# Optimization experiments

Measured on AMD Instinct MI355X. Metric: run time of the kernel, lower is better.

The kernel has to match this reference:

```python
import jax, jax.numpy as jnp
import numpy as np

B, C, H, W = 16, 512, 56, 56
K = 8            # downsample factor
HEADS = 8
EXP = 3          # attn_expansion (int)
HID = HEADS * EXP  # DLA hidden channels = 24
HEAD_DIM = C // HEADS
SCALE = HEAD_DIM ** -0.5
N = H * W
NK = (H // K) * (W // K)
EPS = 1e-5


def conv2d(x, w, stride=1, padding='VALID', groups=1):
    # x: NCHW, w: OIHW
    return jax.lax.conv_general_dilated(
        x, w, (stride, stride), padding,
        dimension_numbers=('NCHW', 'OIHW', 'NCHW'),
        feature_group_count=groups)


def group_norm(x, scale, bias, groups):
    b, c, h, w = x.shape
    xg = x.reshape(b, groups, c // groups, h, w)
    mu = xg.mean(axis=(2, 3, 4), keepdims=True)
    var = xg.var(axis=(2, 3, 4), keepdims=True)
    xg = (xg - mu) * jax.lax.rsqrt(var + EPS)
    x = xg.reshape(b, c, h, w)
    return x * scale[None, :, None, None] + bias[None, :, None, None]


def swish(x):
    return x * jax.nn.sigmoid(x)


def setup_inputs() -> dict:
    key = jax.random.key(0)
    ks = jax.random.split(key, 12)
    s = 0.02
    return {
        'x': jax.random.normal(ks[0], (B, C, H, W), jnp.float32),
        'q_w': jax.random.normal(ks[1], (C, C), jnp.float32) * s,
        'down_w': jax.random.normal(ks[2], (C, 1, K, K), jnp.float32) * s,  # depthwise
        'kv_w': jax.random.normal(ks[3], (C, 2 * C), jnp.float32) * s,
        'proj_w': jax.random.normal(ks[4], (C, C), jnp.float32) * s,
        'proj_b': jnp.zeros((C,), jnp.float32),
        'rel_bias': jax.random.normal(ks[5], (N, NK), jnp.float32) * s,
        'expand_w': jax.random.normal(ks[6], (HID, HEADS, 1, 1), jnp.float32) * s,
        'gn1_s': jnp.ones((HID,), jnp.float32), 'gn1_b': jnp.zeros((HID,), jnp.float32),
        'dw_w': jax.random.normal(ks[7], (HID, 1, 3, 3), jnp.float32) * s,
        'gn2_s': jnp.ones((HID,), jnp.float32), 'gn2_b': jnp.zeros((HID,), jnp.float32),
        'reduce_w': jax.random.normal(ks[8], (HEADS, HID, 1, 1), jnp.float32) * s,
        'gn3_s': jnp.ones((HEADS,), jnp.float32), 'gn3_b': jnp.zeros((HEADS,), jnp.float32),
    }


def dla(a, expand_w, gn1_s, gn1_b, dw_w, gn2_s, gn2_b, reduce_w, gn3_s, gn3_b):
    # a: (B, HEADS, N, NK) treated as NCHW image
    a = swish(group_norm(conv2d(a, expand_w), gn1_s, gn1_b, EXP))
    a = swish(group_norm(conv2d(a, dw_w, padding='SAME', groups=HID), gn2_s, gn2_b, EXP))
    a = group_norm(conv2d(a, reduce_w), gn3_s, gn3_b, 1)
    return a


def reference(x, q_w, down_w, kv_w, proj_w, proj_b, rel_bias,
              expand_w, gn1_s, gn1_b, dw_w, gn2_s, gn2_b,
              reduce_w, gn3_s, gn3_b):
    b = x.shape[0]
    # downsampled kv: depthwise conv kernel=stride=K
    kvx = conv2d(x, down_w, stride=K, groups=C)           # (B, C, H/K, W/K)
    kvx = kvx.reshape(b, C, NK).transpose(0, 2, 1)        # (B, NK, C)
    kv = kvx @ kv_w                                       # (B, NK, 2C)
    kv = kv.reshape(b, NK, 2, HEADS, HEAD_DIM).transpose(2, 0, 3, 1, 4)
    k, v = kv[0], kv[1]                                   # (B, heads, NK, hd)
    q = (x.reshape(b, C, N).transpose(0, 2, 1) @ q_w)     # (B, N, C)
    q = q.reshape(b, N, HEADS, HEAD_DIM).transpose(0, 2, 1, 3)  # (B, heads, N, hd)
    attn = jnp.einsum('bhnd,bhmd->bhnm', q, k) * SCALE + rel_bias
    attn = jax.nn.softmax(attn, axis=-1)
    attn = dla(attn, expand_w, gn1_s, gn1_b, dw_w, gn2_s, gn2_b,
               reduce_w, gn3_s, gn3_b)
    out = jnp.einsum('bhnm,bhmd->bhnd', attn, v)          # (B, heads, N, hd)
    out = out.transpose(0, 2, 1, 3).reshape(b, N, C)      # (B, N, C)
    out = out @ proj_w + proj_b
    # faithful to torch: raw reshape (B, N, C) -> (B, C, H, W), no transpose
    return out.reshape(b, C, H, W)
```

## Files before the change

kernel.cpp:

```cpp
#include <hip/hip_runtime.h>
#include <hip/hip_bf16.h>
#include <stdint.h>

#define B_    16
#define C_    512
#define HIMG  56
#define N_    3136
#define NK_   49
#define NH_   8
#define HD_   64
#define JP_   52
#define J_    416
#define HID_  24
#define MP_   50
#define POS_  153664
#define CNT_  1229312.0f
#define EPS_  1e-5f
#define SCALE_ 0.125f

typedef __attribute__((ext_vector_type(8))) short short8;
typedef __attribute__((ext_vector_type(4))) float floatx4;

static __device__ __forceinline__ uint16_t f2bf(float f) {
  uint32_t u = __builtin_bit_cast(uint32_t, f);
  u = (u + 0x7FFFu + ((u >> 16) & 1u)) >> 16;
  return (uint16_t)u;
}
static __device__ __forceinline__ float bf2f(uint16_t h) {
  uint32_t u = ((uint32_t)h) << 16;
  return __builtin_bit_cast(float, u);
}
static __device__ __forceinline__ uint16_t f2h(float f) {
  _Float16 h = (_Float16)f;
  return __builtin_bit_cast(uint16_t, h);
}
static __device__ __forceinline__ float h2f(uint16_t u) {
  return (float)__builtin_bit_cast(_Float16, u);
}
static __device__ __forceinline__ float swishf(float z) {
  return z * __builtin_amdgcn_rcpf(1.f + __expf(-z));
}
static __device__ __forceinline__ void ld_h8(const uint16_t* p, float* a) {
  uint4 v = *(const uint4*)p;
  a[0] = h2f((uint16_t)(v.x & 0xFFFFu)); a[1] = h2f((uint16_t)(v.x >> 16));
  a[2] = h2f((uint16_t)(v.y & 0xFFFFu)); a[3] = h2f((uint16_t)(v.y >> 16));
  a[4] = h2f((uint16_t)(v.z & 0xFFFFu)); a[5] = h2f((uint16_t)(v.z >> 16));
  a[6] = h2f((uint16_t)(v.w & 0xFFFFu)); a[7] = h2f((uint16_t)(v.w >> 16));
}

static __device__ __forceinline__ void gn1_affine(const float* __restrict__ moms,
    const float* __restrict__ ew, const float* __restrict__ gs,
    const float* __restrict__ gb, int b, int g, float* al, float* be) {
  float m1[8];
#pragma unroll
  for (int h = 0; h < 8; ++h) m1[h] = moms[b * 44 + h];
  float sum = 0.f, ssq = 0.f;
#pragma unroll
  for (int o2 = 0; o2 < 8; ++o2) {
    int o = g * 8 + o2;
    float e[8];
#pragma unroll
    for (int h = 0; h < 8; ++h) e[h] = ew[o * 8 + h];
    float so = 0.f;
#pragma unroll
    for (int h = 0; h < 8; ++h) so += e[h] * m1[h];
    sum += so;
    int idx = 8;
#pragma unroll
    for (int h = 0; h < 8; ++h)
#pragma unroll
      for (int h2 = h; h2 < 8; ++h2) {
        float cf = e[h] * e[h2] * ((h == h2) ? 1.f : 2.f);
        ssq += cf * moms[b * 44 + idx];
        ++idx;
      }
  }
  float mean = sum * (1.f / CNT_);
  float var = ssq * (1.f / CNT_) - mean * mean;
  float inv = rsqrtf(var + EPS_);
#pragma unroll
  for (int o2 = 0; o2 < 8; ++o2) {
    al[o2] = inv * gs[g * 8 + o2];
    be[o2] = gb[g * 8 + o2] - mean * al[o2];
  }
}

__global__ __launch_bounds__(256) void k_kvx(const float* __restrict__ x,
                                             const float* __restrict__ dw,
                                             uint16_t* __restrict__ kvxbf,
                                             uint16_t* __restrict__ xbf) {
  int g = blockIdx.x * 256 + threadIdx.x;
  int b = g / (C_ * NK_);
  int rem = g % (C_ * NK_);
  int c = rem / NK_;
  int m = rem % NK_;
  int ph = m / 7, pw = m % 7;
  const size_t base = ((size_t)(b * C_ + c)) * N_ + (ph * 8) * HIMG + pw * 8;
  const float* xp = x + base;
  uint16_t* xbp = xbf + base;
  const float* wp = dw + c * 64;
  float acc = 0.f;
#pragma unroll
  for (int i = 0; i < 8; ++i) {
    float4 a  = *(const float4*)(xp + i * HIMG);
    float4 bq = *(const float4*)(xp + i * HIMG + 4);
    acc += a.x*wp[i*8+0] + a.y*wp[i*8+1] + a.z*wp[i*8+2] + a.w*wp[i*8+3]
         + bq.x*wp[i*8+4] + bq.y*wp[i*8+5] + bq.z*wp[i*8+6] + bq.w*wp[i*8+7];
    uint32_t q0 = (uint32_t)f2bf(a.x)  | ((uint32_t)f2bf(a.y)  << 16);
    uint32_t q1 = (uint32_t)f2bf(a.z)  | ((uint32_t)f2bf(a.w)  << 16);
    uint32_t q2 = (uint32_t)f2bf(bq.x) | ((uint32_t)f2bf(bq.y) << 16);
    uint32_t q3 = (uint32_t)f2bf(bq.z) | ((uint32_t)f2bf(bq.w) << 16);
    *(uint4*)(xbp + (size_t)i * HIMG) = make_uint4(q0, q1, q2, q3);
  }
  kvxbf[((size_t)(b * NK_ + m)) * C_ + c] = f2bf(acc);
}

__global__ __launch_bounds__(256) void k_kv(const uint16_t* __restrict__ kvxbf,
                                            const float* __restrict__ kv_w,
                                            float* __restrict__ kv) {
  const int ct = blockIdx.x, b = blockIdx.y;
  const int j0 = ct * 64;
  const int tid = threadIdx.x, wvid = tid >> 6, lane = tid & 63;
  __shared__ __align__(16) uint32_t A32[64 * 20];
  __shared__ __align__(16) uint32_t B32[64 * 20];
  floatx4 acc[4];
#pragma unroll
  for (int t = 0; t < 4; ++t) acc[t] = (floatx4){0.f,0.f,0.f,0.f};
  const int am = tid & 63, ak = tid >> 6;
  const int bj = tid & 63, bk = tid >> 6;
  for (int ks = 0; ks < 16; ++ks) {
    const int c0 = ks * 32;
    __syncthreads();
    {
      uint4 av = make_uint4(0, 0, 0, 0);
      if (am < NK_)
        av = *(const uint4*)(kvxbf + ((size_t)(b * NK_ + am)) * C_ + c0 + ak * 8);
      *(uint4*)&A32[am * 20 + ak * 4] = av;
    }
    {
      uint32_t pk[4];
#pragma unroll
      for (int r = 0; r < 4; ++r) {
        float f0 = kv_w[(size_t)(c0 + bk * 8 + 2 * r)     * 1024 + j0 + bj];
        float f1 = kv_w[(size_t)(c0 + bk * 8 + 2 * r + 1) * 1024 + j0 + bj];
        pk[r] = (uint32_t)f2bf(f0) | ((uint32_t)f2bf(f1) << 16);
      }
      *(uint4*)&B32[bj * 20 + bk * 4] = make_uint4(pk[0], pk[1], pk[2], pk[3]);
    }
    __syncthreads();
    short8 af = *(const short8*)&A32[(wvid * 16 + (lane & 15)) * 20 + (lane >> 4) * 4];
#pragma unroll
    for (int t = 0; t < 4; ++t) {
      short8 bfb = *(const short8*)&B32[(t * 16 + (lane & 15)) * 20 + (lane >> 4) * 4];
      acc[t] = __builtin_amdgcn_mfma_f32_16x16x32_bf16(af, bfb, acc[t], 0, 0, 0);
    }
  }
  const int rb = wvid * 16 + ((lane >> 4) << 2), cb = lane & 15;
#pragma unroll
  for (int t = 0; t < 4; ++t)
#pragma unroll
    for (int r2 = 0; r2 < 4; ++r2) {
      int m = rb + r2;
      if (m < NK_)
        kv[((size_t)(b * NK_ + m)) * 1024 + j0 + t * 16 + cb] = acc[t][r2];
    }
}

__global__ __launch_bounds__(256) void k_wqk(const float* __restrict__ kv,
                                             const float* __restrict__ q_w,
                                             uint16_t* __restrict__ wqkT) {
  int b = blockIdx.x, h = blockIdx.y;
  __shared__ float ksm[56 * 64];
  for (int idx = threadIdx.x; idx < 56 * 64; idx += 256) {
    int m = idx >> 6, d = idx & 63;
    ksm[idx] = (m < NK_) ? kv[((size_t)(b * NK_ + m)) * 1024 + h * HD_ + d] : 0.f;
  }
  __syncthreads();
#pragma unroll
  for (int cc = 0; cc < 2; ++cc) {
    int c = threadIdx.x + cc * 256;
    float qrow[64];
    const float* qp = q_w + (size_t)c * C_ + h * HD_;
#pragma unroll
    for (int d = 0; d < 64; ++d) qrow[d] = qp[d];
    for (int mc = 0; mc < NK_; mc += 8) {
      int cnt = min(8, NK_ - mc);
      float acc[8] = {0,0,0,0,0,0,0,0};
      for (int d = 0; d < 64; ++d) {
        float q = qrow[d];
#pragma unroll
        for (int i = 0; i < 8; ++i) acc[i] += q * ksm[(mc + i) * 64 + d];
      }
      for (int i = 0; i < cnt; ++i)
        wqkT[((size_t)(b * J_ + h * JP_ + mc + i)) * C_ + c] = f2bf(acc[i] * SCALE_);
    }
  }
  for (int idx = threadIdx.x; idx < 3 * C_; idx += 256) {
    int rr = idx / C_, c = idx % C_;
    wqkT[((size_t)(b * J_ + h * JP_ + 49 + rr)) * C_ + c] = 0;
  }
}

__global__ __launch_bounds__(256) void k_wv(const float* __restrict__ kv,
                                            const float* __restrict__ proj_w,
                                            uint16_t* __restrict__ wvT) {
  int b = blockIdx.x, h = blockIdx.y;
  __shared__ float vsm[56 * 64];
  for (int idx = threadIdx.x; idx < 56 * 64; idx += 256) {
    int m = idx >> 6, d = idx & 63;
    vsm[idx] = (m < NK_) ? kv[((size_t)(b * NK_ + m)) * 1024 + 512 + h * HD_ + d] : 0.f;
  }
  __syncthreads();
#pragma unroll
  for (int cc = 0; cc < 2; ++cc) {
    int c = threadIdx.x + cc * 256;
    for (int mc = 0; mc < NK_; mc += 8) {
      int cnt = min(8, NK_ - mc);
      float acc[8] = {0,0,0,0,0,0,0,0};
      for (int d = 0; d < 64; ++d) {
        float w = proj_w[(size_t)(h * HD_ + d) * C_ + c];
#pragma unroll
        for (int i = 0; i < 8; ++i) acc[i] += vsm[(mc + i) * 64 + d] * w;
      }
      uint16_t* dst = wvT + ((size_t)(b * C_ + c)) * J_ + h * JP_ + mc;
      if (cnt == 8) {
        uint32_t pk[4];
#pragma unroll
        for (int i = 0; i < 4; ++i)
          pk[i] = (uint32_t)f2bf(acc[2*i]) | ((uint32_t)f2bf(acc[2*i+1]) << 16);
        *(uint2*)(dst)     = make_uint2(pk[0], pk[1]);
        *(uint2*)(dst + 4) = make_uint2(pk[2], pk[3]);
      } else {
        for (int i = 0; i < cnt; ++i) dst[i] = f2bf(acc[i]);
      }
    }
    uint16_t* pd = wvT + ((size_t)(b * C_ + c)) * J_ + h * JP_ + 49;
    pd[0] = 0; pd[1] = 0; pd[2] = 0;
  }
}

__global__ __launch_bounds__(256) void k_attn(const uint16_t* __restrict__ xbf,
                                              const uint16_t* __restrict__ wqkT,
                                              const float* __restrict__ rel_bias,
                                              uint16_t* __restrict__ attn) {
  const int mt = blockIdx.x, ct = blockIdx.y, b = blockIdx.z;
  const int n0 = mt * 64, j0 = ct * 208;
  const int tid = threadIdx.x, wvid = tid >> 6, lane = tid & 63;
  __shared__ __align__(16) char smem[64 * 212 * 4];
  uint32_t* A32 = (uint32_t*)smem;
  uint32_t* B32 = A32 + 64 * 20;
  float* Ss = (float*)smem;

  floatx4 acc[13];
#pragma unroll
  for (int t = 0; t < 13; ++t) acc[t] = (floatx4){0.f,0.f,0.f,0.f};

  const int an = tid & 63, acp = tid >> 6;
  for (int ks = 0; ks < 16; ++ks) {
    const int c0 = ks * 32;
    __syncthreads();
    {
      const uint16_t* xb = xbf + ((size_t)b * C_ + c0 + acp * 8) * N_ + n0 + an;
      uint32_t pk[4];
#pragma unroll
      for (int jj = 0; jj < 4; ++jj) {
        uint32_t f0 = xb[(size_t)(2*jj) * N_];
        uint32_t f1 = xb[(size_t)(2*jj+1) * N_];
        pk[jj] = f0 | (f1 << 16);
      }
      *(uint4*)&A32[an * 20 + acp * 4] = make_uint4(pk[0], pk[1], pk[2], pk[3]);
    }
    for (int idx = tid; idx < 832; idx += 256) {
      int jl = idx >> 2, q = idx & 3;
      uint4 v = *(const uint4*)(wqkT + ((size_t)b * J_ + j0 + jl) * C_ + c0 + q * 8);
      *(uint4*)&B32[jl * 20 + q * 4] = v;
    }
    __syncthreads();
    short8 af = *(const short8*)&A32[(wvid * 16 + (lane & 15)) * 20 + (lane >> 4) * 4];
#pragma unroll
    for (int t = 0; t < 13; ++t) {
      short8 bfb = *(const short8*)&B32[(16 * t + (lane & 15)) * 20 + (lane >> 4) * 4];
      acc[t] = __builtin_amdgcn_mfma_f32_16x16x32_bf16(af, bfb, acc[t], 0, 0, 0);
    }
  }
  __syncthreads();
  {
    const int rb = wvid * 16 + ((lane >> 4) << 2), cb = lane & 15;
#pragma unroll
    for (int t = 0; t < 13; ++t)
#pragma unroll
      for (int r2 = 0; r2 < 4; ++r2)
        Ss[(rb + r2) * 212 + t * 16 + cb] = acc[t][r2];
  }
  __syncthreads();
  {
    const int row = tid >> 2, hh = tid & 3;
    const int n = n0 + row;
    const float* bias = rel_bias + (size_t)n * NK_;
    float* srow = &Ss[row * 212 + hh * JP_];
    float mx = -1e30f;
    for (int m = 0; m < NK_; ++m) mx = fmaxf(mx, srow[m] + bias[m]);
    float sum = 0.f;
    for (int m = 0; m < NK_; ++m) { float e = __expf(srow[m] + bias[m] - mx); srow[m] = e; sum += e; }
    float inv = 1.f / sum;
    for (int m = 0; m < NK_; ++m) srow[m] *= inv;
  }
  __syncthreads();
  for (int task = tid; task < 64 * NK_; task += 256) {
    int row = task / NK_, m = task % NK_;
    const float* sr = &Ss[row * 212];
    uint32_t lo = (uint32_t)f2h(sr[m])        | ((uint32_t)f2h(sr[JP_ + m])     << 16);
    uint32_t hi = (uint32_t)f2h(sr[2*JP_ + m]) | ((uint32_t)f2h(sr[3*JP_ + m]) << 16);
    *(uint2*)(attn + (((size_t)b * N_ + n0 + row) * MP_ + m) * 8 + ct * 4) = make_uint2(lo, hi);
  }
}

__global__ __launch_bounds__(256) void k_moms(const uint16_t* __restrict__ attn,
                                              float* __restrict__ moms) {
  int nt = blockIdx.x, b = blockIdx.y;
  float vals[44];
#pragma unroll
  for (int k = 0; k < 44; ++k) vals[k] = 0.f;
  for (int task = threadIdx.x; task < 64 * NK_; task += 256) {
    int r = task / NK_, m = task % NK_;
    float a[8];
    ld_h8(attn + (((size_t)b * N_ + nt * 64 + r) * MP_ + m) * 8, a);
#pragma unroll
    for (int h = 0; h < 8; ++h) vals[h] += a[h];
    int idx = 8;
#pragma unroll
    for (int h = 0; h < 8; ++h)
#pragma unroll
      for (int h2 = h; h2 < 8; ++h2) { vals[idx] += a[h] * a[h2]; ++idx; }
  }
  __shared__ float red[4][44];
  int lane = threadIdx.x & 63, wvid = threadIdx.x >> 6;
#pragma unroll
  for (int k = 0; k < 44; ++k) {
#pragma unroll
    for (int off = 32; off; off >>= 1) vals[k] += __shfl_down(vals[k], off, 64);
  }
  if (lane == 0) {
#pragma unroll
    for (int k = 0; k < 44; ++k) red[wvid][k] = vals[k];
  }
  __syncthreads();
  if (threadIdx.x < 44) {
    float t = red[0][threadIdx.x] + red[1][threadIdx.x] + red[2][threadIdx.x] + red[3][threadIdx.x];
    atomicAdd(&moms[b * 44 + threadIdx.x], t);
  }
}

__global__ void k_aff(const float* __restrict__ moms, const float* __restrict__ ew,
                      const float* __restrict__ gn1_s, const float* __restrict__ gn1_b,
                      float* __restrict__ gn1ab) {
  int t = threadIdx.x;
  if (t >= 48) return;
  int b = t / 3, g = t % 3;
  float al[8], be[8];
  gn1_affine(moms, ew, gn1_s, gn1_b, b, g, al, be);
#pragma unroll
  for (int o = 0; o < 8; ++o) { gn1ab[t * 16 + o] = al[o]; gn1ab[t * 16 + 8 + o] = be[o]; }
}

__global__ void k_aff2(const float* __restrict__ gn2sums, const float* __restrict__ gn2_s,
                       const float* __restrict__ gn2_b, float* __restrict__ gn2ab) {
  int t = threadIdx.x;
  if (t >= 48) return;
  int b = t / 3, g = t % 3;
  float s2 = gn2sums[b * 6 + g * 2], q2 = gn2sums[b * 6 + g * 2 + 1];
  float mean = s2 * (1.f / CNT_);
  float var = q2 * (1.f / CNT_) - mean * mean;
  float inv = rsqrtf(var + EPS_);
#pragma unroll
  for (int o = 0; o < 8; ++o) {
    float al = inv * gn2_s[g * 8 + o];
    gn2ab[t * 16 + o] = al;
    gn2ab[t * 16 + 8 + o] = gn2_b[g * 8 + o] - mean * al;
  }
}

template<bool STORE>
__global__ __launch_bounds__(256) void k_dla0_t(const uint16_t* __restrict__ attn,
    const float* __restrict__ ew, const float* __restrict__ gn1ab,
    const float* __restrict__ dww, float* __restrict__ gn2sums,
    uint16_t* __restrict__ a2buf) {
  const int nt = blockIdx.x, b = blockIdx.y, g = blockIdx.z;
  const int n0 = nt * 16;
  __shared__ __align__(16) float h1s[18 * 51 * 8];
  __shared__ float red[4][2];
  float al[8], be[8];
  {
    const float* ab = gn1ab + (b * 3 + g) * 16;
#pragma unroll
    for (int o = 0; o < 8; ++o) { al[o] = ab[o]; be[o] = ab[8 + o]; }
  }
  for (int task = threadIdx.x; task < 18 * NK_; task += 256) {
    int r = task / NK_, m = task % NK_;
    int n = n0 - 1 + r;
    float h1v[8];
    if (n < 0 || n >= N_) {
#pragma unroll
      for (int o = 0; o < 8; ++o) h1v[o] = 0.f;
    } else {
      float a[8];
      ld_h8(attn + (((size_t)b * N_ + n) * MP_ + m) * 8, a);
#pragma unroll
      for (int o = 0; o < 8; ++o) {
        float v = 0.f;
#pragma unroll
        for (int h = 0; h < 8; ++h) v += ew[(g * 8 + o) * 8 + h] * a[h];
        h1v[o] = swishf(v * al[o] + be[o]);
      }
    }
    float* dst = &h1s[(r * 51 + m + 1) * 8];
    *(float4*)dst = make_float4(h1v[0], h1v[1], h1v[2], h1v[3]);
    *(float4*)(dst + 4) = make_float4(h1v[4], h1v[5], h1v[6], h1v[7]);
  }
  for (int idx = threadIdx.x; idx < 18 * 16; idx += 256) {
    int r = idx >> 4, c = idx & 15;
    h1s[(r * 51 + (c >> 3) * 50) * 8 + (c & 7)] = 0.f;
  }
  __syncthreads();
  const int row = threadIdx.x >> 4, mg = threadIdx.x & 15;
  const int m0 = mg * 3;
  const int mlim = (mg == 15) ? 4 : 3;
  float a2[4][8];
#pragma unroll
  for (int mi = 0; mi < 4; ++mi)
#pragma unroll
    for (int o = 0; o < 8; ++o) a2[mi][o] = 0.f;
#pragma unroll
  for (int dr = 0; dr < 3; ++dr) {
    float win[48];
    const float* src = &h1s[((row + dr) * 51 + m0) * 8];
#pragma unroll
    for (int k = 0; k < 12; ++k)
      *(float4*)&win[k * 4] = *(const float4*)(src + k * 4);
#pragma unroll
    for (int o = 0; o < 8; ++o) {
      float wa = dww[(g * 8 + o) * 9 + dr * 3 + 0];
      float wb = dww[(g * 8 + o) * 9 + dr * 3 + 1];
      float wc = dww[(g * 8 + o) * 9 + dr * 3 + 2];
#pragma unroll
      for (int mi = 0; mi < 4; ++mi)
        a2[mi][o] += win[mi * 8 + o] * wa + win[(mi + 1) * 8 + o] * wb + win[(mi + 2) * 8 + o] * wc;
    }
  }
  float s0 = 0.f, q0 = 0.f;
#pragma unroll
  for (int mi = 0; mi < 4; ++mi) {
    if (mi < mlim) {
#pragma unroll
      for (int o = 0; o < 8; ++o) { s0 += a2[mi][o]; q0 += a2[mi][o] * a2[mi][o]; }
    }
  }
  int lane = threadIdx.x & 63, wvid = threadIdx.x >> 6;
#pragma unroll
  for (int off = 32; off; off >>= 1) { s0 += __shfl_down(s0, off, 64); q0 += __shfl_down(q0, off, 64); }
  if (lane == 0) { red[wvid][0] = s0; red[wvid][1] = q0; }
  __syncthreads();
  if (threadIdx.x < 2) {
    float t = red[0][threadIdx.x] + red[1][threadIdx.x] + red[2][threadIdx.x] + red[3][threadIdx.x];
    atomicAdd(&gn2sums[b * 6 + g * 2 + threadIdx.x], t);
  }
  if (STORE) {
    uint32_t* a2s = (uint32_t*)h1s;
#pragma unroll
    for (int mi = 0; mi < 4; ++mi) {
      if (mi < mlim) {
        uint32_t pk[4];
#pragma unroll
        for (int q = 0; q < 4; ++q)
          pk[q] = (uint32_t)f2h(a2[mi][2*q]) | ((uint32_t)f2h(a2[mi][2*q+1]) << 16);
        *(uint4*)&a2s[(row * NK_ + m0 + mi) * 4] = make_uint4(pk[0], pk[1], pk[2], pk[3]);
      }
    }
    __syncthreads();
    uint16_t* dstb = a2buf + ((size_t)(b * 3 + g) * POS_ + (size_t)n0 * NK_) * 8;
    for (int idx = threadIdx.x; idx < 16 * NK_; idx += 256)
      *(uint4*)(dstb + (size_t)idx * 8) = *(const uint4*)&a2s[idx * 4];
  }
}

__global__ __launch_bounds__(256) void k_dla1b(const uint16_t* __restrict__ a2buf,
    const float* __restrict__ gn2ab, const float* __restrict__ rww,
    float* __restrict__ gn3sums, uint16_t* __restrict__ rbuf) {
  const int b = blockIdx.y;
  const int pos = blockIdx.x * 256 + threadIdx.x;
  __shared__ float rws[192];
  __shared__ float red[4][2];
  for (int i = threadIdx.x; i < 192; i += 256) rws[i] = rww[i];
  __syncthreads();
  float r[8] = {0.f,0.f,0.f,0.f,0.f,0.f,0.f,0.f};
  if (pos < POS_) {
#pragma unroll
    for (int g = 0; g < 3; ++g) {
      const float* ab = gn2ab + (b * 3 + g) * 16;
      uint4 v = *(const uint4*)(a2buf + ((size_t)(b * 3 + g) * POS_ + pos) * 8);
      uint32_t w[4] = {v.x, v.y, v.z, v.w};
#pragma unroll
      for (int q = 0; q < 4; ++q) {
#pragma unroll
        for (int hl = 0; hl < 2; ++hl) {
          int o = q * 2 + hl;
          float f = h2f((uint16_t)(hl ? (w[q] >> 16) : (w[q] & 0xFFFFu)));
          float sw = swishf(f * ab[o] + ab[8 + o]);
#pragma unroll
          for (int p = 0; p < 8; ++p) r[p] += rws[p * HID_ + g * 8 + o] * sw;
        }
      }
    }
  }
  float sr = 0.f, qr = 0.f;
#pragma unroll
  for (int p = 0; p < 8; ++p) { sr += r[p]; qr += r[p] * r[p]; }
  int lane = threadIdx.x & 63, wvid = threadIdx.x >> 6;
#pragma unroll
  for (int off = 32; off; off >>= 1) { sr += __shfl_down(sr, off, 64); qr += __shfl_down(qr, off, 64); }
  if (lane == 0) { red[wvid][0] = sr; red[wvid][1] = qr; }
  __syncthreads();
  if (threadIdx.x < 2) {
    float t = red[0][threadIdx.x] + red[1][threadIdx.x] + red[2][threadIdx.x] + red[3][threadIdx.x];
    atomicAdd(&gn3sums[b * 2 + threadIdx.x], t);
  }
  if (pos < POS_) {
    int n = pos / NK_, m = pos - n * NK_;
    uint16_t* dst = rbuf + ((size_t)b * N_ + n) * J_;
#pragma unroll
    for (int p = 0; p < 8; ++p) dst[p * JP_ + m] = f2bf(r[p]);
    if (m < 3) {
#pragma unroll
      for (int p = 0; p < 8; ++p) dst[p * JP_ + 49 + m] = 0;
    }
  }
}

__global__ __launch_bounds__(256) void k_dla1s(const uint16_t* __restrict__ attn,
    const float* __restrict__ ew, const float* __restrict__ gn1ab,
    const float* __restrict__ dww, const float* __restrict__ gn2ab,
    const float* __restrict__ rww, float* __restrict__ gn3sums,
    uint16_t* __restrict__ rbuf) {
  const int nt = blockIdx.x, b = blockIdx.y;
  const int n0 = nt * 16;
  __shared__ __align__(16) float h1s[18 * 51 * 8];
  __shared__ float red[4][2];
  const int row = threadIdx.x >> 4, mg = threadIdx.x & 15;
  const int m0 = mg * 3;
  const int mlim = (mg == 15) ? 4 : 3;
  float racc[4][8];
#pragma unroll
  for (int mi = 0; mi < 4; ++mi)
#pragma unroll
    for (int p = 0; p < 8; ++p) racc[mi][p] = 0.f;

  for (int g = 0; g < 3; ++g) {
    float al[8], be[8], al2[8], be2[8];
    {
      const float* ab1 = gn1ab + (b * 3 + g) * 16;
      const float* ab2 = gn2ab + (b * 3 + g) * 16;
#pragma unroll
      for (int o = 0; o < 8; ++o) {
        al[o] = ab1[o]; be[o] = ab1[8 + o];
        al2[o] = ab2[o]; be2[o] = ab2[8 + o];
      }
    }
    __syncthreads();
    for (int task = threadIdx.x; task < 18 * NK_; task += 256) {
      int r = task / NK_, m = task % NK_;
      int n = n0 - 1 + r;
      float h1v[8];
      if (n < 0 || n >= N_) {
#pragma unroll
        for (int o = 0; o < 8; ++o) h1v[o] = 0.f;
      } else {
        float a[8];
        ld_h8(attn + (((size_t)b * N_ + n) * MP_ + m) * 8, a);
#pragma unroll
        for (int o = 0; o < 8; ++o) {
          float v = 0.f;
#pragma unroll
          for (int h = 0; h < 8; ++h) v += ew[(g * 8 + o) * 8 + h] * a[h];
          h1v[o] = swishf(v * al[o] + be[o]);
        }
      }
      float* dst = &h1s[(r * 51 + m + 1) * 8];
      *(float4*)dst = make_float4(h1v[0], h1v[1], h1v[2], h1v[3]);
      *(float4*)(dst + 4) = make_float4(h1v[4], h1v[5], h1v[6], h1v[7]);
    }
    for (int idx = threadIdx.x; idx < 18 * 16; idx += 256) {
      int r = idx >> 4, c = idx & 15;
      h1s[(r * 51 + (c >> 3) * 50) * 8 + (c & 7)] = 0.f;
    }
    __syncthreads();
    float a2[4][8];
#pragma unroll
    for (int mi = 0; mi < 4; ++mi)
#pragma unroll
      for (int o = 0; o < 8; ++o) a2[mi][o] = 0.f;
#pragma unroll
    for (int dr = 0; dr < 3; ++dr) {
      float win[48];
      const float* src = &h1s[((row + dr) * 51 + m0) * 8];
#pragma unroll
      for (int k = 0; k < 12; ++k)
        *(float4*)&win[k * 4] = *(const float4*)(src + k * 4);
#pragma unroll
      for (int o = 0; o < 8; ++o) {
        float wa = dww[(g * 8 + o) * 9 + dr * 3 + 0];
        float wb = dww[(g * 8 + o) * 9 + dr * 3 + 1];
        float wc = dww[(g * 8 + o) * 9 + dr * 3 + 2];
#pragma unroll
        for (int mi = 0; mi < 4; ++mi)
          a2[mi][o] += win[mi * 8 + o] * wa + win[(mi + 1) * 8 + o] * wb + win[(mi + 2) * 8 + o] * wc;
      }
    }
#pragma unroll
    for (int mi = 0; mi < 4; ++mi) {
      if (mi < mlim) {
#pragma unroll
        for (int o = 0; o < 8; ++o) {
          float sw = swishf(a2[mi][o] * al2[o] + be2[o]);
#pragma unroll
          for (int p = 0; p < 8; ++p) racc[mi][p] += rww[p * HID_ + g * 8 + o] * sw;
        }
      }
    }
  }
  float sr = 0.f, qr = 0.f;
  const int n = n0 + row;
  uint16_t* dstbase = rbuf + ((size_t)b * N_ + n) * J_;
#pragma unroll
  for (int mi = 0; mi < 4; ++mi) {
    if (mi < mlim) {
      int m = m0 + mi;
#pragma unroll
      for (int p = 0; p < 8; ++p) {
        float v = racc[mi][p];
        dstbase[p * JP_ + m] = f2bf(v);
        sr += v; qr += v * v;
      }
    }
  }
  if (mg == 15) {
#pragma unroll
    for (int p = 0; p < 8; ++p) {
      dstbase[p * JP_ + 49] = 0; dstbase[p * JP_ + 50] = 0; dstbase[p * JP_ + 51] = 0;
    }
  }
  int lane = threadIdx.x & 63, wvid = threadIdx.x >> 6;
#pragma unroll
  for (int off = 32; off; off >>= 1) { sr += __shfl_down(sr, off, 64); qr += __shfl_down(qr, off, 64); }
  if (lane == 0) { red[wvid][0] = sr; red[wvid][1] = qr; }
  __syncthreads();
  if (threadIdx.x < 2) {
    float t = red[0][threadIdx.x] + red[1][threadIdx.x] + red[2][threadIdx.x] + red[3][threadIdx.x];
    atomicAdd(&gn3sums[b * 2 + threadIdx.x], t);
  }
}

__global__ __launch_bounds__(256) void k_out(const uint16_t* __restrict__ rr,
    const uint16_t* __restrict__ wvT, const float* __restrict__ gn3sums,
    const float* __restrict__ gn3_s, const float* __restrict__ gn3_b,
    const float* __restrict__ proj_b, float* __restrict__ outp) {
  const int mt = blockIdx.x, ct = blockIdx.y, b = blockIdx.z;
  const int n0 = mt * 64, c0 = ct * 128;
  const int tid = threadIdx.x, wvid = tid >> 6, lane = tid & 63;
  __shared__ __align__(16) uint32_t A32[64 * 20];
  __shared__ __align__(16) uint32_t B32[128 * 20];
  __shared__ float ab3[J_ * 2];
  {
    float ssum = gn3sums[b*2], sq = gn3sums[b*2+1];
    float mean = ssum * (1.f / CNT_);
    float var = sq * (1.f / CNT_) - mean * mean;
    float inv = rsqrtf(var + EPS_);
    for (int j = tid; j < J_; j += 256) {
      int h = j / JP_;
      float al = inv * gn3_s[h];
      ab3[j*2] = al; ab3[j*2+1] = gn3_b[h] - mean * al;
    }
  }
  floatx4 acc[8];
#pragma unroll
  for (int t = 0; t < 8; ++t) acc[t] = (floatx4){0.f,0.f,0.f,0.f};
  const int an = tid >> 2, acp = tid & 3;
  for (int ks = 0; ks < 13; ++ks) {
    const int k0 = ks * 32;
    __syncthreads();
    {
      const uint16_t* src = rr + ((size_t)b * N_ + n0 + an) * J_ + k0 + acp * 8;
      uint4 v = *(const uint4*)src;
      uint32_t raw[4] = {v.x, v.y, v.z, v.w};
      uint32_t pk[4];
#pragma unroll
      for (int jj = 0; jj < 4; ++jj) {
        int j = k0 + acp * 8 + jj * 2;
        float f0 = bf2f((uint16_t)(raw[jj] & 0xFFFFu)) * ab3[j*2]     + ab3[j*2+1];
        float f1 = bf2f((uint16_t)(raw[jj] >> 16))     * ab3[(j+1)*2] + ab3[(j+1)*2+1];
        pk[jj] = (uint32_t)f2bf(f0) | ((uint32_t)f2bf(f1) << 16);
      }
      *(uint4*)&A32[an * 20 + acp * 4] = make_uint4(pk[0], pk[1], pk[2], pk[3]);
    }
    for (int idx = tid; idx < 128 * 4; idx += 256) {
      int rw2 = idx >> 2, q = idx & 3;
      uint4 v = *(const uint4*)(wvT + ((size_t)b * C_ + c0 + rw2) * J_ + k0 + q * 8);
      *(uint4*)&B32[rw2 * 20 + q * 4] = v;
    }
    __syncthreads();
    short8 af = *(const short8*)&A32[(wvid * 16 + (lane & 15)) * 20 + (lane >> 4) * 4];
#pragma unroll
    for (int t = 0; t < 8; ++t) {
      short8 bfb = *(const short8*)&B32[(t * 16 + (lane & 15)) * 20 + (lane >> 4) * 4];
      acc[t] = __builtin_amdgcn_mfma_f32_16x16x32_bf16(af, bfb, acc[t], 0, 0, 0);
    }
  }
  const int rb = wvid * 16 + ((lane >> 4) << 2);
#pragma unroll
  for (int t = 0; t < 8; ++t) {
    int c = c0 + t * 16 + (lane & 15);
    float pb = proj_b[c];
#pragma unroll
    for (int r2 = 0; r2 < 4; ++r2)
      outp[((size_t)b * N_ + n0 + rb + r2) * C_ + c] = acc[t][r2] + pb;
  }
}

extern "C" void kernel_launch(void* const* d_in, const int* in_sizes, int n_in,
                              void* d_out, int out_size, void* d_ws, size_t ws_size,
                              hipStream_t stream) {
  (void)in_sizes; (void)n_in; (void)out_size;
  const float* x      = (const float*)d_in[0];
  const float* q_w    = (const float*)d_in[1];
  const float* down_w = (const float*)d_in[2];
  const float* kv_w   = (const float*)d_in[3];
  const float* proj_w = (const float*)d_in[4];
  const float* proj_b = (const float*)d_in[5];
  const float* rel_b  = (const float*)d_in[6];
  const float* ew     = (const float*)d_in[7];
  const float* gn1_s  = (const float*)d_in[8];
  const float* gn1_b  = (const float*)d_in[9];
  const float* dw_w   = (const float*)d_in[10];
  const float* gn2_s  = (const float*)d_in[11];
  const float* gn2_b  = (const float*)d_in[12];
  const float* red_w  = (const float*)d_in[13];
  const float* gn3_s  = (const float*)d_in[14];
  const float* gn3_b  = (const float*)d_in[15];
  float* outp = (float*)d_out;

  const size_t NEED_SMALL = 109176832;
  const size_t NEED_BIG   = 206727168;
  if (ws_size < NEED_SMALL) return;
  const bool big = (ws_size >= NEED_BIG);

  char* ws = (char*)d_ws;
  uint16_t* xbf   = (uint16_t*)(ws);
  uint16_t* kvxbf = (uint16_t*)(ws + 51380224);
  float*    kv    = (float*)(ws + 52183040);
  uint16_t* wqkT  = (uint16_t*)(ws + 55394304);
  uint16_t* a2    = (uint16_t*)(ws);
  uint16_t* attn;
  uint16_t* wvT;
  uint16_t* rbuf;
  float*    stats;
  if (big) {
    attn  = (uint16_t*)(ws + 118013952);
    wvT   = (uint16_t*)(ws + 158154752);
    rbuf  = (uint16_t*)(ws + 164970496);
    stats = (float*)(ws + 206716928);
  } else {
    wvT   = (uint16_t*)(ws + 62210048);
    attn  = (uint16_t*)(ws + 69025792);
    rbuf  = (uint16_t*)(ws);
    stats = (float*)(ws + 109166592);
  }
  float* moms    = stats;
  float* gn2sums = stats + 704;
  float* gn3sums = stats + 800;
  float* gn1ab   = stats + 1024;
  float* gn2ab   = stats + 1792;

  hipMemsetAsync(stats, 0, 4096, stream);
  k_kvx<<<1568, 256, 0, stream>>>(x, down_w, kvxbf, xbf);
  k_kv<<<dim3(16, 16), 256, 0, stream>>>(kvxbf, kv_w, kv);
  k_wqk<<<dim3(16, 8), 256, 0, stream>>>(kv, q_w, wqkT);
  k_wv<<<dim3(16, 8), 256, 0, stream>>>(kv, proj_w, wvT);
  k_attn<<<dim3(49, 2, 16), 256, 0, stream>>>(xbf, wqkT, rel_b, attn);
  k_moms<<<dim3(49, 16), 256, 0, stream>>>(attn, moms);
  k_aff<<<1, 64, 0, stream>>>(moms, ew, gn1_s, gn1_b, gn1ab);
  if (big) {
    k_dla0_t<true><<<dim3(196, 16, 3), 256, 0, stream>>>(attn, ew, gn1ab, dw_w,
                                                         gn2sums, a2);
    k_aff2<<<1, 64, 0, stream>>>(gn2sums, gn2_s, gn2_b, gn2ab);
    k_dla1b<<<dim3(601, 16), 256, 0, stream>>>(a2, gn2ab, red_w, gn3sums, rbuf);
  } else {
    k_dla0_t<false><<<dim3(196, 16, 3), 256, 0, stream>>>(attn, ew, gn1ab, dw_w,
                                                          gn2sums, nullptr);
    k_aff2<<<1, 64, 0, stream>>>(gn2sums, gn2_s, gn2_b, gn2ab);
    k_dla1s<<<dim3(196, 16), 256, 0, stream>>>(attn, ew, gn1ab, dw_w, gn2ab,
                                               red_w, gn3sums, rbuf);
  }
  k_out<<<dim3(49, 4, 16), 256, 0, stream>>>(rbuf, wvT, gn3sums, gn3_s, gn3_b, proj_b, outp);
}
```

Before: 782.3 us.

## Do attention softmax in registers and split attn buffer into unpadded head-half planes

The QK^T kernel now pads each head's key block to 64 columns so that each wave holds four whole heads in MFMA accumulators. The bias add and softmax run in registers with cross-lane shuffles, which removes the shared-memory score spill and the serial per-row softmax loops. The A operand is loaded straight into registers instead of being staged through LDS. The attention buffer drops the 50-entry m padding and is stored as two planes of four heads each, and the downstream readers now do two 8-byte loads instead of one 16-byte load. The cost is more zero-padded MFMA work on the padded columns and the rewritten buffer offsets.

```diff
diff --git a/kernel.cpp b/kernel.cpp
--- a/kernel.cpp
+++ b/kernel.cpp
@@ -11,9 +11,11 @@
 #define HD_   64
 #define JP_   52
 #define J_    416
+#define JPQ_  64
+#define JQ_   512
 #define HID_  24
-#define MP_   50
 #define POS_  153664
+#define PLH_  9834496
 #define CNT_  1229312.0f
 #define EPS_  1e-5f
 #define SCALE_ 0.125f
@@ -40,12 +42,14 @@
 static __device__ __forceinline__ float swishf(float z) {
   return z * __builtin_amdgcn_rcpf(1.f + __expf(-z));
 }
-static __device__ __forceinline__ void ld_h8(const uint16_t* p, float* a) {
-  uint4 v = *(const uint4*)p;
-  a[0] = h2f((uint16_t)(v.x & 0xFFFFu)); a[1] = h2f((uint16_t)(v.x >> 16));
-  a[2] = h2f((uint16_t)(v.y & 0xFFFFu)); a[3] = h2f((uint16_t)(v.y >> 16));
-  a[4] = h2f((uint16_t)(v.z & 0xFFFFu)); a[5] = h2f((uint16_t)(v.z >> 16));
-  a[6] = h2f((uint16_t)(v.w & 0xFFFFu)); a[7] = h2f((uint16_t)(v.w >> 16));
+static __device__ __forceinline__ void ld_attn8(const uint16_t* __restrict__ attn,
+                                                size_t off, float* a) {
+  uint2 v0 = *(const uint2*)(attn + off);
+  uint2 v1 = *(const uint2*)(attn + PLH_ + off);
+  a[0] = h2f((uint16_t)(v0.x & 0xFFFFu)); a[1] = h2f((uint16_t)(v0.x >> 16));
+  a[2] = h2f((uint16_t)(v0.y & 0xFFFFu)); a[3] = h2f((uint16_t)(v0.y >> 16));
+  a[4] = h2f((uint16_t)(v1.x & 0xFFFFu)); a[5] = h2f((uint16_t)(v1.x >> 16));
+  a[6] = h2f((uint16_t)(v1.y & 0xFFFFu)); a[7] = h2f((uint16_t)(v1.y >> 16));
 }
 
 static __device__ __forceinline__ void gn1_affine(const float* __restrict__ moms,
@@ -192,12 +196,12 @@
         for (int i = 0; i < 8; ++i) acc[i] += q * ksm[(mc + i) * 64 + d];
       }
       for (int i = 0; i < cnt; ++i)
-        wqkT[((size_t)(b * J_ + h * JP_ + mc + i)) * C_ + c] = f2bf(acc[i] * SCALE_);
-    }
-  }
-  for (int idx = threadIdx.x; idx < 3 * C_; idx += 256) {
+        wqkT[((size_t)(b * JQ_ + h * JPQ_ + mc + i)) * C_ + c] = f2bf(acc[i] * SCALE_);
+    }
+  }
+  for (int idx = threadIdx.x; idx < 15 * C_; idx += 256) {
     int rr = idx / C_, c = idx % C_;
-    wqkT[((size_t)(b * J_ + h * JP_ + 49 + rr)) * C_ + c] = 0;
+    wqkT[((size_t)(b * JQ_ + h * JPQ_ + 49 + rr)) * C_ + c] = 0;
   }
 }
 
@@ -244,75 +248,96 @@
                                               const float* __restrict__ rel_bias,
                                               uint16_t* __restrict__ attn) {
   const int mt = blockIdx.x, ct = blockIdx.y, b = blockIdx.z;
-  const int n0 = mt * 64, j0 = ct * 208;
+  const int n0 = mt * 64, jb = ct * 256;
   const int tid = threadIdx.x, wvid = tid >> 6, lane = tid & 63;
-  __shared__ __align__(16) char smem[64 * 212 * 4];
-  uint32_t* A32 = (uint32_t*)smem;
-  uint32_t* B32 = A32 + 64 * 20;
-  float* Ss = (float*)smem;
-
-  floatx4 acc[13];
-#pragma unroll
-  for (int t = 0; t < 13; ++t) acc[t] = (floatx4){0.f,0.f,0.f,0.f};
-
-  const int an = tid & 63, acp = tid >> 6;
+  __shared__ __align__(16) char smem[25088 + 64 * 52 * 4];
+  uint32_t* B32 = (uint32_t*)smem;
+  uint16_t* eS  = (uint16_t*)smem;
+  float* biasS  = (float*)(smem + 25088);
+
+  for (int idx = tid; idx < 64 * NK_; idx += 256) {
+    int r = idx / NK_, m = idx - r * NK_;
+    biasS[r * 52 + m] = rel_bias[(size_t)(n0 + r) * NK_ + m];
+  }
+
+  floatx4 acc[16];
+#pragma unroll
+  for (int t = 0; t < 16; ++t) acc[t] = (floatx4){0.f,0.f,0.f,0.f};
+
+  const int arow = n0 + (wvid << 4) + (lane & 15);
+  const int acg = (lane >> 4) << 3;
   for (int ks = 0; ks < 16; ++ks) {
     const int c0 = ks * 32;
     __syncthreads();
+    for (int idx = tid; idx < 1024; idx += 256) {
+      int jl = idx >> 2, q = idx & 3;
+      uint4 v = *(const uint4*)(wqkT + ((size_t)(b * JQ_ + jb + jl)) * C_ + c0 + q * 8);
+      *(uint4*)&B32[jl * 20 + q * 4] = v;
+    }
+    union { uint32_t u[4]; short8 s8; } A;
     {
-      const uint16_t* xb = xbf + ((size_t)b * C_ + c0 + acp * 8) * N_ + n0 + an;
-      uint32_t pk[4];
+      const uint16_t* xb = xbf + ((size_t)(b * C_ + c0 + acg)) * N_ + arow;
 #pragma unroll
       for (int jj = 0; jj < 4; ++jj) {
-        uint32_t f0 = xb[(size_t)(2*jj) * N_];
-        uint32_t f1 = xb[(size_t)(2*jj+1) * N_];
-        pk[jj] = f0 | (f1 << 16);
-      }
-      *(uint4*)&A32[an * 20 + acp * 4] = make_uint4(pk[0], pk[1], pk[2], pk[3]);
-    }
-    for (int idx = tid; idx < 832; idx += 256) {
-      int jl = idx >> 2, q = idx & 3;
-      uint4 v = *(const uint4*)(wqkT + ((size_t)b * J_ + j0 + jl) * C_ + c0 + q * 8);
-      *(uint4*)&B32[jl * 20 + q * 4] = v;
+        uint32_t f0 = xb[(size_t)(2 * jj) * N_];
+        uint32_t f1 = xb[(size_t)(2 * jj + 1) * N_];
+        A.u[jj] = f0 | (f1 << 16);
+      }
     }
     __syncthreads();
-    short8 af = *(const short8*)&A32[(wvid * 16 + (lane & 15)) * 20 + (lane >> 4) * 4];
-#pragma unroll
-    for (int t = 0; t < 13; ++t) {
-      short8 bfb = *(const short8*)&B32[(16 * t + (lane & 15)) * 20 + (lane >> 4) * 4];
-      acc[t] = __builtin_amdgcn_mfma_f32_16x16x32_bf16(af, bfb, acc[t], 0, 0, 0);
-    }
-  }
-  __syncthreads();
-  {
-    const int rb = wvid * 16 + ((lane >> 4) << 2), cb = lane & 15;
-#pragma unroll
-    for (int t = 0; t < 13; ++t)
-#pragma unroll
-      for (int r2 = 0; r2 < 4; ++r2)
-        Ss[(rb + r2) * 212 + t * 16 + cb] = acc[t][r2];
-  }
-  __syncthreads();
-  {
-    const int row = tid >> 2, hh = tid & 3;
-    const int n = n0 + row;
-    const float* bias = rel_bias + (size_t)n * NK_;
-    float* srow = &Ss[row * 212 + hh * JP_];
-    float mx = -1e30f;
-    for (int m = 0; m < NK_; ++m) mx = fmaxf(mx, srow[m] + bias[m]);
-    float sum = 0.f;
-    for (int m = 0; m < NK_; ++m) { float e = __expf(srow[m] + bias[m] - mx); srow[m] = e; sum += e; }
-    float inv = 1.f / sum;
-    for (int m = 0; m < NK_; ++m) srow[m] *= inv;
-  }
-  __syncthreads();
-  for (int task = tid; task < 64 * NK_; task += 256) {
-    int row = task / NK_, m = task % NK_;
-    const float* sr = &Ss[row * 212];
-    uint32_t lo = (uint32_t)f2h(sr[m])        | ((uint32_t)f2h(sr[JP_ + m])     << 16);
-    uint32_t hi = (uint32_t)f2h(sr[2*JP_ + m]) | ((uint32_t)f2h(sr[3*JP_ + m]) << 16);
-    *(uint2*)(attn + (((size_t)b * N_ + n0 + row) * MP_ + m) * 8 + ct * 4) = make_uint2(lo, hi);
-  }
+#pragma unroll
+    for (int t = 0; t < 16; ++t) {
+      short8 bfb = *(const short8*)&B32[(t * 16 + (lane & 15)) * 20 + (lane >> 4) * 4];
+      acc[t] = __builtin_amdgcn_mfma_f32_16x16x32_bf16(A.s8, bfb, acc[t], 0, 0, 0);
+    }
+  }
+  __syncthreads();
+
+  const int rbase = (wvid << 4) + ((lane >> 4) << 2);
+  const int cb = lane & 15;
+#pragma unroll
+  for (int hh = 0; hh < 4; ++hh) {
+#pragma unroll
+    for (int r2 = 0; r2 < 4; ++r2) {
+      const float* bs = &biasS[(rbase + r2) * 52];
+      float v0 = acc[hh*4+0][r2] + bs[cb];
+      float v1 = acc[hh*4+1][r2] + bs[16 + cb];
+      float v2 = acc[hh*4+2][r2] + bs[32 + cb];
+      float v3 = (cb == 0) ? (acc[hh*4+3][r2] + bs[48]) : -1e30f;
+      float mx = fmaxf(fmaxf(v0, v1), fmaxf(v2, v3));
+      mx = fmaxf(mx, __shfl_xor(mx, 1));
+      mx = fmaxf(mx, __shfl_xor(mx, 2));
+      mx = fmaxf(mx, __shfl_xor(mx, 4));
+      mx = fmaxf(mx, __shfl_xor(mx, 8));
+      float e0 = __expf(v0 - mx), e1 = __expf(v1 - mx), e2 = __expf(v2 - mx);
+      float e3 = (cb == 0) ? __expf(v3 - mx) : 0.f;
+      float s = e0 + e1 + e2 + e3;
+      s += __shfl_xor(s, 1);
+      s += __shfl_xor(s, 2);
+      s += __shfl_xor(s, 4);
+      s += __shfl_xor(s, 8);
+      float inv = __builtin_amdgcn_rcpf(s);
+      acc[hh*4+0][r2] = e0 * inv;
+      acc[hh*4+1][r2] = e1 * inv;
+      acc[hh*4+2][r2] = e2 * inv;
+      acc[hh*4+3][r2] = e3 * inv;
+    }
+  }
+#pragma unroll
+  for (int hh = 0; hh < 4; ++hh)
+#pragma unroll
+    for (int tt = 0; tt < 4; ++tt) {
+      int m = tt * 16 + cb;
+      if (m < NK_) {
+#pragma unroll
+        for (int r2 = 0; r2 < 4; ++r2)
+          eS[((rbase + r2) * NK_ + m) * 4 + hh] = f2h(acc[hh*4+tt][r2]);
+      }
+    }
+  __syncthreads();
+  uint16_t* dst = attn + (size_t)ct * PLH_ + ((size_t)b * N_ + n0) * NK_ * 4;
+  for (int idx = tid; idx < 64 * NK_; idx += 256)
+    *(uint2*)(dst + idx * 4) = *(const uint2*)&eS[idx * 4];
 }
 
 __global__ __launch_bounds__(256) void k_moms(const uint16_t* __restrict__ attn,
@@ -322,9 +347,8 @@
 #pragma unroll
   for (int k = 0; k < 44; ++k) vals[k] = 0.f;
   for (int task = threadIdx.x; task < 64 * NK_; task += 256) {
-    int r = task / NK_, m = task % NK_;
     float a[8];
-    ld_h8(attn + (((size_t)b * N_ + nt * 64 + r) * MP_ + m) * 8, a);
+    ld_attn8(attn, ((size_t)b * N_ + nt * 64) * NK_ * 4 + (size_t)task * 4, a);
 #pragma unroll
     for (int h = 0; h < 8; ++h) vals[h] += a[h];
     int idx = 8;
@@ -404,7 +428,7 @@
       for (int o = 0; o < 8; ++o) h1v[o] = 0.f;
     } else {
       float a[8];
-      ld_h8(attn + (((size_t)b * N_ + n) * MP_ + m) * 8, a);
+      ld_attn8(attn, (((size_t)b * N_ + n) * NK_ + m) * 4, a);
 #pragma unroll
       for (int o = 0; o < 8; ++o) {
         float v = 0.f;
@@ -575,7 +599,7 @@
         for (int o = 0; o < 8; ++o) h1v[o] = 0.f;
       } else {
         float a[8];
-        ld_h8(attn + (((size_t)b * N_ + n) * MP_ + m) * 8, a);
+        ld_attn8(attn, (((size_t)b * N_ + n) * NK_ + m) * 4, a);
 #pragma unroll
         for (int o = 0; o < 8; ++o) {
           float v = 0.f;
@@ -747,8 +771,8 @@
   const float* gn3_b  = (const float*)d_in[15];
   float* outp = (float*)d_out;
 
-  const size_t NEED_SMALL = 109176832;
-  const size_t NEED_BIG   = 206727168;
+  const size_t NEED_SMALL = 109946880;
+  const size_t NEED_BIG   = 205924352;
   if (ws_size < NEED_SMALL) return;
   const bool big = (ws_size >= NEED_BIG);
 
@@ -764,14 +788,14 @@
   float*    stats;
   if (big) {
     attn  = (uint16_t*)(ws + 118013952);
-    wvT   = (uint16_t*)(ws + 158154752);
-    rbuf  = (uint16_t*)(ws + 164970496);
-    stats = (float*)(ws + 206716928);
+    wvT   = (uint16_t*)(ws + 157351936);
+    rbuf  = (uint16_t*)(ws + 164167680);
+    stats = (float*)(ws + 205914112);
   } else {
-    wvT   = (uint16_t*)(ws + 62210048);
-    attn  = (uint16_t*)(ws + 69025792);
+    wvT   = (uint16_t*)(ws + 63782912);
+    attn  = (uint16_t*)(ws + 70598656);
     rbuf  = (uint16_t*)(ws);
-    stats = (float*)(ws + 109166592);
+    stats = (float*)(ws + 109936640);
   }
   float* moms    = stats;
   float* gn2sums = stats + 704;
```

Result: slower. 798.5 us (+2.1%).

## Split attn buffer into two head-half planes and merge wqk/wv kernels

Applied to the files above, without the earlier changes.

The attention probability buffer moves from an interleaved 8-head layout padded to 50 keys per row to two contiguous planes of 4 heads each, unpadded at 49 keys. The attention kernel now writes each half-tile contiguously, and readers load two 8-byte chunks, one from each plane. Separately, the k_wqk and k_wv kernels are merged into one launch along a z dimension, so the two small projections run concurrently and one launch is saved. Workspace offsets are recomputed, which risks overlap errors if any offset is wrong.

```diff
diff --git a/kernel.cpp b/kernel.cpp
--- a/kernel.cpp
+++ b/kernel.cpp
@@ -12,8 +12,8 @@
 #define JP_   52
 #define J_    416
 #define HID_  24
-#define MP_   50
 #define POS_  153664
+#define PLH_  9834496
 #define CNT_  1229312.0f
 #define EPS_  1e-5f
 #define SCALE_ 0.125f
@@ -40,12 +40,14 @@
 static __device__ __forceinline__ float swishf(float z) {
   return z * __builtin_amdgcn_rcpf(1.f + __expf(-z));
 }
-static __device__ __forceinline__ void ld_h8(const uint16_t* p, float* a) {
-  uint4 v = *(const uint4*)p;
-  a[0] = h2f((uint16_t)(v.x & 0xFFFFu)); a[1] = h2f((uint16_t)(v.x >> 16));
-  a[2] = h2f((uint16_t)(v.y & 0xFFFFu)); a[3] = h2f((uint16_t)(v.y >> 16));
-  a[4] = h2f((uint16_t)(v.z & 0xFFFFu)); a[5] = h2f((uint16_t)(v.z >> 16));
-  a[6] = h2f((uint16_t)(v.w & 0xFFFFu)); a[7] = h2f((uint16_t)(v.w >> 16));
+static __device__ __forceinline__ void ld_attn8(const uint16_t* __restrict__ attn,
+                                                size_t off, float* a) {
+  uint2 v0 = *(const uint2*)(attn + off);
+  uint2 v1 = *(const uint2*)(attn + PLH_ + off);
+  a[0] = h2f((uint16_t)(v0.x & 0xFFFFu)); a[1] = h2f((uint16_t)(v0.x >> 16));
+  a[2] = h2f((uint16_t)(v0.y & 0xFFFFu)); a[3] = h2f((uint16_t)(v0.y >> 16));
+  a[4] = h2f((uint16_t)(v1.x & 0xFFFFu)); a[5] = h2f((uint16_t)(v1.x >> 16));
+  a[6] = h2f((uint16_t)(v1.y & 0xFFFFu)); a[7] = h2f((uint16_t)(v1.y >> 16));
 }
 
 static __device__ __forceinline__ void gn1_affine(const float* __restrict__ moms,
@@ -166,76 +168,74 @@
     }
 }
 
-__global__ __launch_bounds__(256) void k_wqk(const float* __restrict__ kv,
-                                             const float* __restrict__ q_w,
-                                             uint16_t* __restrict__ wqkT) {
+__global__ __launch_bounds__(256) void k_wqkv(const float* __restrict__ kv,
+                                              const float* __restrict__ q_w,
+                                              const float* __restrict__ proj_w,
+                                              uint16_t* __restrict__ wqkT,
+                                              uint16_t* __restrict__ wvT) {
   int b = blockIdx.x, h = blockIdx.y;
-  __shared__ float ksm[56 * 64];
-  for (int idx = threadIdx.x; idx < 56 * 64; idx += 256) {
-    int m = idx >> 6, d = idx & 63;
-    ksm[idx] = (m < NK_) ? kv[((size_t)(b * NK_ + m)) * 1024 + h * HD_ + d] : 0.f;
-  }
-  __syncthreads();
-#pragma unroll
-  for (int cc = 0; cc < 2; ++cc) {
-    int c = threadIdx.x + cc * 256;
-    float qrow[64];
-    const float* qp = q_w + (size_t)c * C_ + h * HD_;
-#pragma unroll
-    for (int d = 0; d < 64; ++d) qrow[d] = qp[d];
-    for (int mc = 0; mc < NK_; mc += 8) {
-      int cnt = min(8, NK_ - mc);
-      float acc[8] = {0,0,0,0,0,0,0,0};
-      for (int d = 0; d < 64; ++d) {
-        float q = qrow[d];
-#pragma unroll
-        for (int i = 0; i < 8; ++i) acc[i] += q * ksm[(mc + i) * 64 + d];
-      }
-      for (int i = 0; i < cnt; ++i)
-        wqkT[((size_t)(b * J_ + h * JP_ + mc + i)) * C_ + c] = f2bf(acc[i] * SCALE_);
-    }
-  }
-  for (int idx = threadIdx.x; idx < 3 * C_; idx += 256) {
-    int rr = idx / C_, c = idx % C_;
-    wqkT[((size_t)(b * J_ + h * JP_ + 49 + rr)) * C_ + c] = 0;
-  }
-}
-
-__global__ __launch_bounds__(256) void k_wv(const float* __restrict__ kv,
-                                            const float* __restrict__ proj_w,
-                                            uint16_t* __restrict__ wvT) {
-  int b = blockIdx.x, h = blockIdx.y;
-  __shared__ float vsm[56 * 64];
-  for (int idx = threadIdx.x; idx < 56 * 64; idx += 256) {
-    int m = idx >> 6, d = idx & 63;
-    vsm[idx] = (m < NK_) ? kv[((size_t)(b * NK_ + m)) * 1024 + 512 + h * HD_ + d] : 0.f;
-  }
-  __syncthreads();
-#pragma unroll
-  for (int cc = 0; cc < 2; ++cc) {
-    int c = threadIdx.x + cc * 256;
-    for (int mc = 0; mc < NK_; mc += 8) {
-      int cnt = min(8, NK_ - mc);
-      float acc[8] = {0,0,0,0,0,0,0,0};
-      for (int d = 0; d < 64; ++d) {
-        float w = proj_w[(size_t)(h * HD_ + d) * C_ + c];
-#pragma unroll
-        for (int i = 0; i < 8; ++i) acc[i] += vsm[(mc + i) * 64 + d] * w;
-      }
-      uint16_t* dst = wvT + ((size_t)(b * C_ + c)) * J_ + h * JP_ + mc;
-      if (cnt == 8) {
-        uint32_t pk[4];
-#pragma unroll
-        for (int i = 0; i < 4; ++i)
-          pk[i] = (uint32_t)f2bf(acc[2*i]) | ((uint32_t)f2bf(acc[2*i+1]) << 16);
-        *(uint2*)(dst)     = make_uint2(pk[0], pk[1]);
-        *(uint2*)(dst + 4) = make_uint2(pk[2], pk[3]);
-      } else {
-        for (int i = 0; i < cnt; ++i) dst[i] = f2bf(acc[i]);
-      }
-    }
-    uint16_t* pd = wvT + ((size_t)(b * C_ + c)) * J_ + h * JP_ + 49;
-    pd[0] = 0; pd[1] = 0; pd[2] = 0;
+  __shared__ float sm[56 * 64];
+  if (blockIdx.z == 0) {
+    for (int idx = threadIdx.x; idx < 56 * 64; idx += 256) {
+      int m = idx >> 6, d = idx & 63;
+      sm[idx] = (m < NK_) ? kv[((size_t)(b * NK_ + m)) * 1024 + h * HD_ + d] : 0.f;
+    }
+    __syncthreads();
+#pragma unroll
+    for (int cc = 0; cc < 2; ++cc) {
+      int c = threadIdx.x + cc * 256;
+      float qrow[64];
+      const float* qp = q_w + (size_t)c * C_ + h * HD_;
+#pragma unroll
+      for (int d = 0; d < 64; ++d) qrow[d] = qp[d];
+      for (int mc = 0; mc < NK_; mc += 8) {
+        int cnt = min(8, NK_ - mc);
+        float acc[8] = {0,0,0,0,0,0,0,0};
+        for (int d = 0; d < 64; ++d) {
+          float q = qrow[d];
+#pragma unroll
+          for (int i = 0; i < 8; ++i) acc[i] += q * sm[(mc + i) * 64 + d];
+        }
+        for (int i = 0; i < cnt; ++i)
+          wqkT[((size_t)(b * J_ + h * JP_ + mc + i)) * C_ + c] = f2bf(acc[i] * SCALE_);
+      }
+    }
+    for (int idx = threadIdx.x; idx < 3 * C_; idx += 256) {
+      int rr = idx / C_, c = idx % C_;
+      wqkT[((size_t)(b * J_ + h * JP_ + 49 + rr)) * C_ + c] = 0;
+    }
+  } else {
+    for (int idx = threadIdx.x; idx < 56 * 64; idx += 256) {
+      int m = idx >> 6, d = idx & 63;
+      sm[idx] = (m < NK_) ? kv[((size_t)(b * NK_ + m)) * 1024 + 512 + h * HD_ + d] : 0.f;
+    }
+    __syncthreads();
+#pragma unroll
+    for (int cc = 0; cc < 2; ++cc) {
+      int c = threadIdx.x + cc * 256;
+      for (int mc = 0; mc < NK_; mc += 8) {
+        int cnt = min(8, NK_ - mc);
+        float acc[8] = {0,0,0,0,0,0,0,0};
+        for (int d = 0; d < 64; ++d) {
+          float w = proj_w[(size_t)(h * HD_ + d) * C_ + c];
+#pragma unroll
+          for (int i = 0; i < 8; ++i) acc[i] += sm[(mc + i) * 64 + d] * w;
+        }
+        uint16_t* dst = wvT + ((size_t)(b * C_ + c)) * J_ + h * JP_ + mc;
+        if (cnt == 8) {
+          uint32_t pk[4];
+#pragma unroll
+          for (int i = 0; i < 4; ++i)
+            pk[i] = (uint32_t)f2bf(acc[2*i]) | ((uint32_t)f2bf(acc[2*i+1]) << 16);
+          *(uint2*)(dst)     = make_uint2(pk[0], pk[1]);
+          *(uint2*)(dst + 4) = make_uint2(pk[2], pk[3]);
+        } else {
+          for (int i = 0; i < cnt; ++i) dst[i] = f2bf(acc[i]);
+        }
+      }
+      uint16_t* pd = wvT + ((size_t)(b * C_ + c)) * J_ + h * JP_ + 49;
+      pd[0] = 0; pd[1] = 0; pd[2] = 0;
+    }
   }
 }
 
@@ -260,7 +260,7 @@
     const int c0 = ks * 32;
     __syncthreads();
     {
-      const uint16_t* xb = xbf + ((size_t)b * C_ + c0 + acp * 8) * N_ + n0 + an;
+      const uint16_t* xb = xbf + ((size_t)(b * C_ + c0 + acp * 8)) * N_ + n0 + an;
       uint32_t pk[4];
 #pragma unroll
       for (int jj = 0; jj < 4; ++jj) {
@@ -306,12 +306,13 @@
     for (int m = 0; m < NK_; ++m) srow[m] *= inv;
   }
   __syncthreads();
+  uint16_t* dst = attn + (size_t)ct * PLH_ + ((size_t)b * N_ + n0) * NK_ * 4;
   for (int task = tid; task < 64 * NK_; task += 256) {
     int row = task / NK_, m = task % NK_;
     const float* sr = &Ss[row * 212];
-    uint32_t lo = (uint32_t)f2h(sr[m])        | ((uint32_t)f2h(sr[JP_ + m])     << 16);
+    uint32_t lo = (uint32_t)f2h(sr[m])         | ((uint32_t)f2h(sr[JP_ + m])   << 16);
     uint32_t hi = (uint32_t)f2h(sr[2*JP_ + m]) | ((uint32_t)f2h(sr[3*JP_ + m]) << 16);
-    *(uint2*)(attn + (((size_t)b * N_ + n0 + row) * MP_ + m) * 8 + ct * 4) = make_uint2(lo, hi);
+    *(uint2*)(dst + (size_t)task * 4) = make_uint2(lo, hi);
   }
 }
 
@@ -322,9 +323,8 @@
 #pragma unroll
   for (int k = 0; k < 44; ++k) vals[k] = 0.f;
   for (int task = threadIdx.x; task < 64 * NK_; task += 256) {
-    int r = task / NK_, m = task % NK_;
     float a[8];
-    ld_h8(attn + (((size_t)b * N_ + nt * 64 + r) * MP_ + m) * 8, a);
+    ld_attn8(attn, ((size_t)b * N_ + nt * 64) * NK_ * 4 + (size_t)task * 4, a);
 #pragma unroll
     for (int h = 0; h < 8; ++h) vals[h] += a[h];
     int idx = 8;
@@ -404,7 +404,7 @@
       for (int o = 0; o < 8; ++o) h1v[o] = 0.f;
     } else {
       float a[8];
-      ld_h8(attn + (((size_t)b * N_ + n) * MP_ + m) * 8, a);
+      ld_attn8(attn, (((size_t)b * N_ + n) * NK_ + m) * 4, a);
 #pragma unroll
       for (int o = 0; o < 8; ++o) {
         float v = 0.f;
@@ -575,7 +575,7 @@
         for (int o = 0; o < 8; ++o) h1v[o] = 0.f;
       } else {
         float a[8];
-        ld_h8(attn + (((size_t)b * N_ + n) * MP_ + m) * 8, a);
+        ld_attn8(attn, (((size_t)b * N_ + n) * NK_ + m) * 4, a);
 #pragma unroll
         for (int o = 0; o < 8; ++o) {
           float v = 0.f;
@@ -747,8 +747,8 @@
   const float* gn3_b  = (const float*)d_in[15];
   float* outp = (float*)d_out;
 
-  const size_t NEED_SMALL = 109176832;
-  const size_t NEED_BIG   = 206727168;
+  const size_t NEED_SMALL = 109946880;
+  const size_t NEED_BIG   = 205924352;
   if (ws_size < NEED_SMALL) return;
   const bool big = (ws_size >= NEED_BIG);
 
@@ -764,14 +764,14 @@
   float*    stats;
   if (big) {
     attn  = (uint16_t*)(ws + 118013952);
-    wvT   = (uint16_t*)(ws + 158154752);
-    rbuf  = (uint16_t*)(ws + 164970496);
-    stats = (float*)(ws + 206716928);
+    wvT   = (uint16_t*)(ws + 157351936);
+    rbuf  = (uint16_t*)(ws + 164167680);
+    stats = (float*)(ws + 205914112);
   } else {
-    wvT   = (uint16_t*)(ws + 62210048);
-    attn  = (uint16_t*)(ws + 69025792);
+    wvT   = (uint16_t*)(ws + 63782912);
+    attn  = (uint16_t*)(ws + 70598656);
     rbuf  = (uint16_t*)(ws);
-    stats = (float*)(ws + 109166592);
+    stats = (float*)(ws + 109936640);
   }
   float* moms    = stats;
   float* gn2sums = stats + 704;
@@ -782,8 +782,7 @@
   hipMemsetAsync(stats, 0, 4096, stream);
   k_kvx<<<1568, 256, 0, stream>>>(x, down_w, kvxbf, xbf);
   k_kv<<<dim3(16, 16), 256, 0, stream>>>(kvxbf, kv_w, kv);
-  k_wqk<<<dim3(16, 8), 256, 0, stream>>>(kv, q_w, wqkT);
-  k_wv<<<dim3(16, 8), 256, 0, stream>>>(kv, proj_w, wvT);
+  k_wqkv<<<dim3(16, 8, 2), 256, 0, stream>>>(kv, q_w, proj_w, wqkT, wvT);
   k_attn<<<dim3(49, 2, 16), 256, 0, stream>>>(xbf, wqkT, rel_b, attn);
   k_moms<<<dim3(49, 16), 256, 0, stream>>>(attn, moms);
   k_aff<<<1, 64, 0, stream>>>(moms, ew, gn1_s, gn1_b, gn1ab);
```

Result: faster. 722.5 us (-7.6%).
